# Kernel tuning notes

Hardware: AMD Instinct MI355X
Metric: run time of the kernel (lower is better)

## Reference

```python
import jax, jax.numpy as jnp
import numpy as np

B = 1024           # number of drug pairs (graphs per side)
ATOMS = 64         # atoms per molecule
N = B * ATOMS      # total atoms per side
H = 512            # hidden_size * number_of_molecules
FFN_H = 2048
OUT = 86           # num_tasks


def setup_inputs() -> dict:
    key = jax.random.key(0)
    ks = jax.random.split(key, 12)
    inv = 1.0 / np.sqrt(H)
    inv2 = 1.0 / np.sqrt(2 * H)
    invf = 1.0 / np.sqrt(FFN_H)
    return {
        "left_output": jax.random.normal(ks[0], (B, H), jnp.float32),
        "right_output": jax.random.normal(ks[1], (B, H), jnp.float32),
        "left_atom": jax.random.normal(ks[2], (N, H), jnp.float32),
        "right_atom": jax.random.normal(ks[3], (N, H), jnp.float32),
        "left_batch": jnp.arange(N, dtype=jnp.int32) // ATOMS,
        "right_batch": jnp.arange(N, dtype=jnp.int32) // ATOMS,
        "noise": jax.random.uniform(ks[4], (B, H), jnp.float32),
        "w_i_w": jax.random.normal(ks[5], (H, H), jnp.float32) * inv,
        "w_i_b": jnp.zeros((H,), jnp.float32),
        "prj_i_w": jax.random.normal(ks[6], (H, H), jnp.float32) * inv,
        "prj_i_b": jnp.zeros((H,), jnp.float32),
        "ffn1_w": jax.random.normal(ks[7], (2 * H, FFN_H), jnp.float32) * inv2,
        "ffn1_b": jnp.zeros((FFN_H,), jnp.float32),
        "ffn2_w": jax.random.normal(ks[8], (FFN_H, OUT), jnp.float32) * invf,
        "ffn2_b": jnp.zeros((OUT,), jnp.float32),
    }


def _seg_softmax(s, seg, num_segments):
    m = jax.ops.segment_max(s, seg, num_segments=num_segments)
    e = jnp.exp(s - m[seg])
    z = jax.ops.segment_sum(e, seg, num_segments=num_segments)
    return e / z[seg]


def reference(left_output, right_output, left_atom, right_atom,
              left_batch, right_batch, noise,
              w_i_w, w_i_b, prj_i_w, prj_i_b,
              ffn1_w, ffn1_b, ffn2_w, ffn2_b):
    # repeat_interleave(left_output, degree(right_batch)) == gather by segment id
    left_align = left_output[right_batch]    # [N_r, H]
    right_align = right_output[left_batch]   # [N_l, H]

    # cross-molecule coattention scores (elementwise product + reduce)
    left_scores = jnp.sum((left_atom @ w_i_w + w_i_b) * (right_align @ prj_i_w + prj_i_b), axis=-1)
    left_scores = _seg_softmax(left_scores, left_batch, B)
    right_scores = jnp.sum((right_atom @ w_i_w + w_i_b) * (left_align @ prj_i_w + prj_i_b), axis=-1)
    right_scores = _seg_softmax(right_scores, right_batch, B)

    # attention-weighted global add pool
    h_output = jax.ops.segment_sum(left_atom * right_align * left_scores[:, None], left_batch, num_segments=B)
    t_output = jax.ops.segment_sum(right_atom * left_align * right_scores[:, None], right_batch, num_segments=B)

    # sign-directed noise perturbation (same noise for both sides, as in original)
    nrm = jnp.maximum(jnp.linalg.norm(noise, axis=-1, keepdims=True), 1e-12)
    noise_n = noise / nrm
    h_pert = h_output + jnp.sign(h_output) * noise_n * 0.1
    t_pert = t_output + jnp.sign(t_output) * noise_n * 0.1

    pair = jnp.concatenate([h_pert, t_pert], axis=-1)  # [B, 2H]
    hid = jax.nn.relu(pair @ ffn1_w + ffn1_b)
    output = hid @ ffn2_w + ffn2_b  # training mode: raw logits, no sigmoid
    return (output, h_output, h_pert, left_scores, right_scores, left_output, right_output)
```

## Files before the change

kernel.cpp:

```cpp
#include <hip/hip_runtime.h>
#include <hip/hip_bf16.h>
#include <float.h>

#define B_ 1024
#define H_ 512
#define N_ (B_ * 64)
#define FFN_ 2048
#define OUT_ 86

typedef __bf16 bf16_t;
typedef __attribute__((ext_vector_type(8))) __bf16 bf16x8;
typedef __attribute__((ext_vector_type(4))) float f32x4;

__device__ __forceinline__ float wred_sum(float v) {
#pragma unroll
  for (int m = 32; m; m >>= 1) v += __shfl_xor(v, m);
  return v;
}
__device__ __forceinline__ float wred_max(float v) {
#pragma unroll
  for (int m = 32; m; m >>= 1) v = fmaxf(v, __shfl_xor(v, m));
  return v;
}

__device__ __forceinline__ void gload_lds16(const void* g, void* l) {
  __builtin_amdgcn_global_load_lds((const __attribute__((address_space(1))) unsigned int*)g,
                                   (__attribute__((address_space(3))) unsigned int*)l, 16, 0, 0);
}

__global__ void k_prep(const float* __restrict__ w_i_w, const float* __restrict__ prj_b,
                       float* __restrict__ dv) {
  int k = blockIdx.x, l = threadIdx.x;
  float s = 0.f;
  for (int h = l; h < H_; h += 64) s += w_i_w[k * H_ + h] * prj_b[h];
  s = wred_sum(s);
  if (l == 0) dv[k] = s;
}

template <bool BT, bool BIAS>
__global__ __launch_bounds__(256) void gemm64(const float* __restrict__ A1, const float* __restrict__ A2,
                                              int M1, const float* __restrict__ Bm,
                                              const float* __restrict__ bias, float* __restrict__ C,
                                              int N, int K) {
  __shared__ float As[16][68];
  __shared__ float Bs[16][68];
  const int bm = blockIdx.x * 64, bn = blockIdx.y * 64;
  const float* __restrict__ A = (bm < M1) ? (A1 + (size_t)bm * K) : (A2 + (size_t)(bm - M1) * K);
  const int t = threadIdx.x;
  const int tx = t & 15, ty = t >> 4;
  float acc[4][4] = {};
  for (int k0 = 0; k0 < K; k0 += 16) {
#pragma unroll
    for (int i = 0; i < 4; i++) {
      int m = (t >> 4) + i * 16;
      As[t & 15][m] = A[(size_t)m * K + k0 + (t & 15)];
    }
    if (BT) {
#pragma unroll
      for (int i = 0; i < 4; i++) {
        int n = (t >> 4) + i * 16;
        Bs[t & 15][n] = Bm[(size_t)(bn + n) * K + k0 + (t & 15)];
      }
    } else {
#pragma unroll
      for (int i = 0; i < 4; i++) {
        int kk = (t >> 6) + i * 4;
        Bs[kk][t & 63] = Bm[(size_t)(k0 + kk) * N + bn + (t & 63)];
      }
    }
    __syncthreads();
#pragma unroll
    for (int kk = 0; kk < 16; kk++) {
      float4 av = *(const float4*)&As[kk][ty * 4];
      float4 bv = *(const float4*)&Bs[kk][tx * 4];
      float a_[4] = {av.x, av.y, av.z, av.w};
      float b_[4] = {bv.x, bv.y, bv.z, bv.w};
#pragma unroll
      for (int i = 0; i < 4; i++)
#pragma unroll
        for (int j = 0; j < 4; j++) acc[i][j] += a_[i] * b_[j];
    }
    __syncthreads();
  }
#pragma unroll
  for (int i = 0; i < 4; i++) {
    int m = bm + ty * 4 + i;
    float tmp[4];
#pragma unroll
    for (int j = 0; j < 4; j++) {
      float x = acc[i][j];
      if (BIAS) x += bias[bn + tx * 4 + j];
      tmp[j] = x;
    }
    float4 v;
    v.x = tmp[0]; v.y = tmp[1]; v.z = tmp[2]; v.w = tmp[3];
    *(float4*)&C[(size_t)m * N + bn + tx * 4] = v;
  }
}

__global__ __launch_bounds__(256) void k_atoms8(const float* __restrict__ atomL, const float* __restrict__ atomR,
                                                const float* __restrict__ uLR,
                                                float* __restrict__ scoresL, float* __restrict__ scoresR,
                                                float* __restrict__ pL, float* __restrict__ pR) {
  const int pair = blockIdx.x;
  const int side = pair >> 10, b = pair & 1023;
  const int t = threadIdx.x, wave = t >> 6, lane = t & 63;

  __shared__ float s_all[64];
  __shared__ float s_nrm[64];

  const float* __restrict__ atom = side ? atomR : atomL;
  const float* __restrict__ u = uLR + (size_t)pair * H_;
  f32x4 u0 = *(const f32x4*)&u[lane * 4];
  f32x4 u1 = *(const f32x4*)&u[256 + lane * 4];

  const float* __restrict__ base = atom + ((size_t)b * 64 + wave * 16) * H_;
  float d[16];
#pragma unroll
  for (int i = 0; i < 16; i++) {
    const float* rp = base + (size_t)i * H_;
    f32x4 x0 = *(const f32x4*)(rp + lane * 4);
    f32x4 x1 = *(const f32x4*)(rp + 256 + lane * 4);
    d[i] = x0.x * u0.x + x0.y * u0.y + x0.z * u0.z + x0.w * u0.w +
           x1.x * u1.x + x1.y * u1.y + x1.z * u1.z + x1.w * u1.w;
  }
#pragma unroll
  for (int i = 0; i < 16; i++) d[i] = wred_sum(d[i]);
  if (lane < 16) {
    float myv = 0.f;
#pragma unroll
    for (int i = 0; i < 16; i++) myv = (lane == i) ? d[i] : myv;
    s_all[wave * 16 + lane] = myv;
  }
  __syncthreads();

  float sv = s_all[lane];
  float M = wred_max(sv);
  float e = __expf(sv - M);
  float Z = wred_sum(e);
  float w_n = e / Z;
  if (wave == 0) {
    s_nrm[lane] = w_n;
    (side ? scoresR : scoresL)[(size_t)b * 64 + lane] = w_n;
  }
  __syncthreads();

  const float* __restrict__ ab = atom + (size_t)b * 64 * H_;
  float q0 = 0.f, q1 = 0.f;
#pragma unroll 8
  for (int r = 0; r < 64; r++) {
    const float w = s_nrm[r];
    q0 += w * ab[(size_t)r * H_ + t];
    q1 += w * ab[(size_t)r * H_ + t + 256];
  }
  float* p = (side ? pR : pL) + (size_t)b * H_;
  p[t] = q0;
  p[t + 256] = q1;
}

__global__ __launch_bounds__(512) void k_pert(const float* __restrict__ lo, const float* __restrict__ ro,
                                              const float* __restrict__ noise,
                                              const float* __restrict__ pL, const float* __restrict__ pR,
                                              float* __restrict__ h_out, float* __restrict__ h_pert,
                                              bf16_t* __restrict__ pairbf) {
  const int b = blockIdx.x, t = threadIdx.x;
  float nv = noise[(size_t)b * H_ + t];
  float sq = nv * nv;
  sq = wred_sum(sq);
  __shared__ float red[8];
  if ((t & 63) == 0) red[t >> 6] = sq;
  __syncthreads();
  float tot = 0.f;
#pragma unroll
  for (int i = 0; i < 8; i++) tot += red[i];
  float nrm = fmaxf(sqrtf(tot), 1e-12f);
  float nn = nv / nrm * 0.1f;
  float h = ro[(size_t)b * H_ + t] * pL[(size_t)b * H_ + t];
  float tt = lo[(size_t)b * H_ + t] * pR[(size_t)b * H_ + t];
  float sh = (h > 0.f) ? 1.f : ((h < 0.f) ? -1.f : 0.f);
  float st = (tt > 0.f) ? 1.f : ((tt < 0.f) ? -1.f : 0.f);
  float hp = h + sh * nn;
  float tp = tt + st * nn;
  h_out[(size_t)b * H_ + t] = h;
  h_pert[(size_t)b * H_ + t] = hp;
  pairbf[(size_t)b * 1024 + t] = (bf16_t)hp;
  pairbf[(size_t)b * 1024 + 512 + t] = (bf16_t)tp;
}

__global__ __launch_bounds__(256) void k_w1t(const float* __restrict__ W1, bf16_t* __restrict__ W1t) {
  __shared__ float tile[32][33];
  const int bx = blockIdx.x;
  const int by = blockIdx.y;
  const int tx = threadIdx.x & 31, ty = threadIdx.x >> 5;
#pragma unroll
  for (int i = ty; i < 32; i += 8)
    tile[i][tx] = W1[(size_t)(by * 32 + i) * FFN_ + bx * 32 + tx];
  __syncthreads();
#pragma unroll
  for (int i = ty; i < 32; i += 8)
    W1t[(size_t)(bx * 32 + i) * 1024 + by * 32 + tx] = (bf16_t)tile[tx][i];
}

__global__ __launch_bounds__(256) void k_ffn1(const bf16_t* __restrict__ Abf, const bf16_t* __restrict__ Bt,
                                              const float* __restrict__ bias, float* __restrict__ C) {
  __shared__ bf16_t As[64 * 64];
  __shared__ bf16_t Bs[64 * 64];
  const int bm = blockIdx.x * 64, bn = blockIdx.y * 64;
  const int t = threadIdx.x;
  const int lane = t & 63, wave = t >> 6;
  const int wm = wave & 1, wn = wave >> 1;
  const int l15 = lane & 15, l4 = lane >> 4;
  f32x4 acc[2][2] = {{{0.f, 0.f, 0.f, 0.f}, {0.f, 0.f, 0.f, 0.f}},
                     {{0.f, 0.f, 0.f, 0.f}, {0.f, 0.f, 0.f, 0.f}}};

  for (int k0 = 0; k0 < 1024; k0 += 64) {
#pragma unroll
    for (int r = 0; r < 2; r++) {
      const int off = (r * 256 + t) * 16;
      const int row = off >> 7;
      const int g = (off >> 4) & 7;
      const int scb = ((g ^ (row & 7)) << 4);
      gload_lds16((const char*)Abf + (size_t)(bm + row) * 2048 + k0 * 2 + scb, (char*)As + off);
      gload_lds16((const char*)Bt + (size_t)(bn + row) * 2048 + k0 * 2 + scb, (char*)Bs + off);
    }
    __syncthreads();
#pragma unroll
    for (int ks = 0; ks < 2; ks++) {
      const int ar0 = wm * 32 + l15, ar1 = ar0 + 16;
      const int br0 = wn * 32 + l15, br1 = br0 + 16;
      const int gA = ks * 4 + l4;
      bf16x8 a0 = *(const bf16x8*)((const char*)As + ar0 * 128 + ((gA ^ (ar0 & 7)) << 4));
      bf16x8 a1 = *(const bf16x8*)((const char*)As + ar1 * 128 + ((gA ^ (ar1 & 7)) << 4));
      bf16x8 b0 = *(const bf16x8*)((const char*)Bs + br0 * 128 + ((gA ^ (br0 & 7)) << 4));
      bf16x8 b1 = *(const bf16x8*)((const char*)Bs + br1 * 128 + ((gA ^ (br1 & 7)) << 4));
      acc[0][0] = __builtin_amdgcn_mfma_f32_16x16x32_bf16(a0, b0, acc[0][0], 0, 0, 0);
      acc[0][1] = __builtin_amdgcn_mfma_f32_16x16x32_bf16(a0, b1, acc[0][1], 0, 0, 0);
      acc[1][0] = __builtin_amdgcn_mfma_f32_16x16x32_bf16(a1, b0, acc[1][0], 0, 0, 0);
      acc[1][1] = __builtin_amdgcn_mfma_f32_16x16x32_bf16(a1, b1, acc[1][1], 0, 0, 0);
    }
    __syncthreads();
  }
#pragma unroll
  for (int mi = 0; mi < 2; mi++)
#pragma unroll
    for (int nj = 0; nj < 2; nj++)
#pragma unroll
      for (int r = 0; r < 4; r++) {
        const int m = bm + wm * 32 + mi * 16 + l4 * 4 + r;
        const int n = bn + wn * 32 + nj * 16 + l15;
        float v = acc[mi][nj][r] + bias[n];
        C[(size_t)m * FFN_ + n] = fmaxf(v, 0.f);
      }
}

__global__ void k_w2t(const float* __restrict__ W2, float* __restrict__ W2t) {
  int idx = blockIdx.x * 256 + threadIdx.x;
  if (idx < OUT_ * FFN_) {
    int n = idx / FFN_, k = idx % FFN_;
    W2t[idx] = W2[(size_t)k * OUT_ + n];
  }
}

__global__ __launch_bounds__(256) void k_ffn2(const float* __restrict__ hid, const float* __restrict__ W2t,
                                              const float* __restrict__ b2, float* __restrict__ out) {
  const int b0 = blockIdx.x * 2;
  const int t = threadIdx.x, wave = t >> 6, lane = t & 63;
  float4 h0[8], h1[8];
  const float* r0 = hid + (size_t)b0 * FFN_;
#pragma unroll
  for (int j = 0; j < 8; j++) {
    h0[j] = *(const float4*)&r0[lane * 4 + j * 256];
    h1[j] = *(const float4*)&r0[FFN_ + lane * 4 + j * 256];
  }
  for (int n = wave; n < OUT_; n += 4) {
    const float* wrow = W2t + (size_t)n * FFN_;
    float s0 = 0.f, s1 = 0.f;
#pragma unroll
    for (int j = 0; j < 8; j++) {
      float4 w4 = *(const float4*)&wrow[lane * 4 + j * 256];
      s0 += w4.x * h0[j].x + w4.y * h0[j].y + w4.z * h0[j].z + w4.w * h0[j].w;
      s1 += w4.x * h1[j].x + w4.y * h1[j].y + w4.z * h1[j].z + w4.w * h1[j].w;
    }
    s0 = wred_sum(s0);
    s1 = wred_sum(s1);
    if (lane == 0) {
      out[(size_t)b0 * OUT_ + n] = s0 + b2[n];
      out[(size_t)(b0 + 1) * OUT_ + n] = s1 + b2[n];
    }
  }
}

extern "C" void kernel_launch(void* const* d_in, const int* in_sizes, int n_in,
                              void* d_out, int out_size, void* d_ws, size_t ws_size,
                              hipStream_t stream) {
  const float* lo = (const float*)d_in[0];
  const float* ro = (const float*)d_in[1];
  const float* la = (const float*)d_in[2];
  const float* ra = (const float*)d_in[3];
  const float* noise = (const float*)d_in[6];
  const float* w_i_w = (const float*)d_in[7];
  const float* prj_w = (const float*)d_in[9];
  const float* prj_b = (const float*)d_in[10];
  const float* W1 = (const float*)d_in[11];
  const float* b1 = (const float*)d_in[12];
  const float* W2 = (const float*)d_in[13];
  const float* b2 = (const float*)d_in[14];

  float* out = (float*)d_out;
  float* o_logits = out;
  float* o_hout  = out + 88064;
  float* o_hpert = o_hout + 524288;
  float* o_ls    = o_hpert + 524288;
  float* o_rs    = o_ls + 65536;
  float* o_lo    = o_rs + 65536;
  float* o_ro    = o_lo + 524288;

  float* ws = (float*)d_ws;
  float* Mt   = ws; ws += 512 * 512;
  float* uLR  = ws; ws += 2048 * 512;
  float* pL   = ws; ws += B_ * H_;
  float* pR   = ws; ws += B_ * H_;
  float* hid  = ws; ws += B_ * FFN_;
  float* W2t  = ws; ws += OUT_ * FFN_;
  bf16_t* pairbf = (bf16_t*)ws; ws += B_ * 1024 / 2;
  bf16_t* W1t    = (bf16_t*)ws; ws += FFN_ * 1024 / 2;
  float* dv   = ws; ws += 512;

  k_prep<<<512, 64, 0, stream>>>(w_i_w, prj_b, dv);
  gemm64<true, false><<<dim3(8, 8), 256, 0, stream>>>(w_i_w, w_i_w, 1 << 30, prj_w, nullptr, Mt, 512, 512);
  gemm64<true, true><<<dim3(32, 8), 256, 0, stream>>>(ro, lo, 1024, Mt, dv, uLR, 512, 512);
  k_w1t<<<dim3(64, 32), 256, 0, stream>>>(W1, W1t);
  k_atoms8<<<2048, 256, 0, stream>>>(la, ra, uLR, o_ls, o_rs, pL, pR);
  k_pert<<<1024, 512, 0, stream>>>(lo, ro, noise, pL, pR, o_hout, o_hpert, pairbf);
  k_ffn1<<<dim3(16, 32), 256, 0, stream>>>(pairbf, W1t, b1, hid);
  k_w2t<<<688, 256, 0, stream>>>(W2, W2t);
  k_ffn2<<<512, 256, 0, stream>>>(hid, W2t, b2, o_logits);
  hipMemcpyAsync(o_lo, lo, (size_t)B_ * H_ * 4, hipMemcpyDeviceToDevice, stream);
  hipMemcpyAsync(o_ro, ro, (size_t)B_ * H_ * 4, hipMemcpyDeviceToDevice, stream);
}
```

Before: 200.1 us.

## Keep atom tiles in registers for pooling and reorder score-vector GEMMs

The atom kernel now loads each wave's 16 atom rows into registers once with explicit batched loads. It reuses them for both the score dot products and the softmax-weighted pooling, then reduces the per-wave partial sums through shared memory. This avoids reading the 64x512 atom block from global memory a second time, at the cost of high register pressure (launch bounds request 2 blocks per SM). The host side also drops the weight-product precompute and bias-dot kernel. It instead computes T = align@prj_w + b and then T@w_i_w^T, which removes two launches but makes the second GEMM larger.

Result: faster. 163.3 us (-18.4%).

```diff
diff --git a/kernel.cpp b/kernel.cpp
--- a/kernel.cpp
+++ b/kernel.cpp
@@ -26,15 +26,6 @@
 __device__ __forceinline__ void gload_lds16(const void* g, void* l) {
   __builtin_amdgcn_global_load_lds((const __attribute__((address_space(1))) unsigned int*)g,
                                    (__attribute__((address_space(3))) unsigned int*)l, 16, 0, 0);
-}
-
-__global__ void k_prep(const float* __restrict__ w_i_w, const float* __restrict__ prj_b,
-                       float* __restrict__ dv) {
-  int k = blockIdx.x, l = threadIdx.x;
-  float s = 0.f;
-  for (int h = l; h < H_; h += 64) s += w_i_w[k * H_ + h] * prj_b[h];
-  s = wred_sum(s);
-  if (l == 0) dv[k] = s;
 }
 
 template <bool BT, bool BIAS>
@@ -98,32 +89,40 @@
   }
 }
 
-__global__ __launch_bounds__(256) void k_atoms8(const float* __restrict__ atomL, const float* __restrict__ atomR,
-                                                const float* __restrict__ uLR,
-                                                float* __restrict__ scoresL, float* __restrict__ scoresR,
-                                                float* __restrict__ pL, float* __restrict__ pR) {
+__global__ __launch_bounds__(256, 2) void k_atoms9(const float* __restrict__ atomL, const float* __restrict__ atomR,
+                                                   const float* __restrict__ uLR,
+                                                   float* __restrict__ scoresL, float* __restrict__ scoresR,
+                                                   float* __restrict__ pL, float* __restrict__ pR) {
   const int pair = blockIdx.x;
   const int side = pair >> 10, b = pair & 1023;
   const int t = threadIdx.x, wave = t >> 6, lane = t & 63;
 
   __shared__ float s_all[64];
   __shared__ float s_nrm[64];
+  __shared__ float pp[4][512];
 
   const float* __restrict__ atom = side ? atomR : atomL;
   const float* __restrict__ u = uLR + (size_t)pair * H_;
   f32x4 u0 = *(const f32x4*)&u[lane * 4];
   f32x4 u1 = *(const f32x4*)&u[256 + lane * 4];
 
-  const float* __restrict__ base = atom + ((size_t)b * 64 + wave * 16) * H_;
+  const float* __restrict__ base = atom + ((size_t)b * 64 + wave * 16) * H_ + lane * 4;
+
+  f32x4 A0[16], A1[16];
+#pragma unroll
+  for (int i = 0; i < 16; i++) {
+    const float* r0 = base + (size_t)i * H_;
+    asm volatile("global_load_dwordx4 %0, %1, off" : "=&v"(A0[i]) : "v"(r0) : "memory");
+    asm volatile("global_load_dwordx4 %0, %1, off" : "=&v"(A1[i]) : "v"(r0 + 256) : "memory");
+  }
+  asm volatile("s_waitcnt vmcnt(0)" ::: "memory");
+  __builtin_amdgcn_sched_barrier(0);
+
   float d[16];
 #pragma unroll
-  for (int i = 0; i < 16; i++) {
-    const float* rp = base + (size_t)i * H_;
-    f32x4 x0 = *(const f32x4*)(rp + lane * 4);
-    f32x4 x1 = *(const f32x4*)(rp + 256 + lane * 4);
-    d[i] = x0.x * u0.x + x0.y * u0.y + x0.z * u0.z + x0.w * u0.w +
-           x1.x * u1.x + x1.y * u1.y + x1.z * u1.z + x1.w * u1.w;
-  }
+  for (int i = 0; i < 16; i++)
+    d[i] = A0[i].x * u0.x + A0[i].y * u0.y + A0[i].z * u0.z + A0[i].w * u0.w +
+           A1[i].x * u1.x + A1[i].y * u1.y + A1[i].z * u1.z + A1[i].w * u1.w;
 #pragma unroll
   for (int i = 0; i < 16; i++) d[i] = wred_sum(d[i]);
   if (lane < 16) {
@@ -134,28 +133,35 @@
   }
   __syncthreads();
 
-  float sv = s_all[lane];
-  float M = wred_max(sv);
-  float e = __expf(sv - M);
-  float Z = wred_sum(e);
-  float w_n = e / Z;
-  if (wave == 0) {
-    s_nrm[lane] = w_n;
-    (side ? scoresR : scoresL)[(size_t)b * 64 + lane] = w_n;
-  }
-  __syncthreads();
-
-  const float* __restrict__ ab = atom + (size_t)b * 64 * H_;
-  float q0 = 0.f, q1 = 0.f;
-#pragma unroll 8
-  for (int r = 0; r < 64; r++) {
-    const float w = s_nrm[r];
-    q0 += w * ab[(size_t)r * H_ + t];
-    q1 += w * ab[(size_t)r * H_ + t + 256];
-  }
+  {
+    float sv = s_all[lane];
+    float M = wred_max(sv);
+    float e = __expf(sv - M);
+    float Z = wred_sum(e);
+    float w_n = e / Z;
+    if (wave == 0) {
+      s_nrm[lane] = w_n;
+      (side ? scoresR : scoresL)[(size_t)b * 64 + lane] = w_n;
+    }
+  }
+  __syncthreads();
+
+  f32x4 q0 = {0.f, 0.f, 0.f, 0.f}, q1 = {0.f, 0.f, 0.f, 0.f};
+#pragma unroll
+  for (int i = 0; i < 16; i++) {
+    const float w = s_nrm[wave * 16 + i];
+    q0.x += w * A0[i].x; q0.y += w * A0[i].y; q0.z += w * A0[i].z; q0.w += w * A0[i].w;
+    q1.x += w * A1[i].x; q1.y += w * A1[i].y; q1.z += w * A1[i].z; q1.w += w * A1[i].w;
+  }
+  *(f32x4*)&pp[wave][lane * 4] = q0;
+  *(f32x4*)&pp[wave][256 + lane * 4] = q1;
+  __syncthreads();
+
+  float v0 = pp[0][t] + pp[1][t] + pp[2][t] + pp[3][t];
+  float v1 = pp[0][t + 256] + pp[1][t + 256] + pp[2][t + 256] + pp[3][t + 256];
   float* p = (side ? pR : pL) + (size_t)b * H_;
-  p[t] = q0;
-  p[t + 256] = q1;
+  p[t] = v0;
+  p[t + 256] = v1;
 }
 
 __global__ __launch_bounds__(512) void k_pert(const float* __restrict__ lo, const float* __restrict__ ro,
@@ -316,7 +322,7 @@
   float* o_ro    = o_lo + 524288;
 
   float* ws = (float*)d_ws;
-  float* Mt   = ws; ws += 512 * 512;
+  float* T    = ws; ws += 2048 * 512;
   float* uLR  = ws; ws += 2048 * 512;
   float* pL   = ws; ws += B_ * H_;
   float* pR   = ws; ws += B_ * H_;
@@ -324,13 +330,11 @@
   float* W2t  = ws; ws += OUT_ * FFN_;
   bf16_t* pairbf = (bf16_t*)ws; ws += B_ * 1024 / 2;
   bf16_t* W1t    = (bf16_t*)ws; ws += FFN_ * 1024 / 2;
-  float* dv   = ws; ws += 512;
-
-  k_prep<<<512, 64, 0, stream>>>(w_i_w, prj_b, dv);
-  gemm64<true, false><<<dim3(8, 8), 256, 0, stream>>>(w_i_w, w_i_w, 1 << 30, prj_w, nullptr, Mt, 512, 512);
-  gemm64<true, true><<<dim3(32, 8), 256, 0, stream>>>(ro, lo, 1024, Mt, dv, uLR, 512, 512);
+
+  gemm64<false, true><<<dim3(32, 8), 256, 0, stream>>>(ro, lo, 1024, prj_w, prj_b, T, 512, 512);
+  gemm64<true, false><<<dim3(32, 8), 256, 0, stream>>>(T, T, 1 << 30, w_i_w, nullptr, uLR, 512, 512);
   k_w1t<<<dim3(64, 32), 256, 0, stream>>>(W1, W1t);
-  k_atoms8<<<2048, 256, 0, stream>>>(la, ra, uLR, o_ls, o_rs, pL, pR);
+  k_atoms9<<<2048, 256, 0, stream>>>(la, ra, uLR, o_ls, o_rs, pL, pR);
   k_pert<<<1024, 512, 0, stream>>>(lo, ro, noise, pL, pR, o_hout, o_hpert, pairbf);
   k_ffn1<<<dim3(16, 32), 256, 0, stream>>>(pairbf, W1t, b1, hid);
   k_w2t<<<688, 256, 0, stream>>>(W2, W2t);
```
